# Kernel optimization log

Hardware: AMD Instinct MI355X
Metric: run time of the kernel (lower is better)

Reference implementation:

```python
import jax, jax.numpy as jnp
import numpy as np

B = 32768      # number of sets
N = 131072     # total elements
DIM = 128      # feature dim
HID = 64       # hidden dim
MAXP = 17      # max_n + 1 (one-hot positional dim / size-class count)


def _ln(x, g, b, eps=1e-5):
    m = jnp.mean(x, -1, keepdims=True)
    v = jnp.var(x, -1, keepdims=True)
    return (x - m) * jax.lax.rsqrt(v + eps) * g + b


def _mlp_ln(x, w1, b1, g, bt, w2, b2):
    return jnp.tanh(_ln(x @ w1 + b1, g, bt)) @ w2 + b2


def _mlp(x, w1, b1, w2, b2):
    return jnp.tanh(x @ w1 + b1) @ w2 + b2


def _lin_init(key, fan_in, fan_out):
    k1, k2 = jax.random.split(key)
    s = 1.0 / np.sqrt(fan_in)
    return (jax.random.uniform(k1, (fan_in, fan_out), jnp.float32, -s, s),
            jax.random.uniform(k2, (fan_out,), jnp.float32, -s, s))


def setup_inputs() -> dict:
    key = jax.random.key(0)
    ks = jax.random.split(key, 16)
    inp = {}
    inp['x'] = jax.random.normal(ks[0], (N, DIM), jnp.float32)
    inp['batch'] = jnp.sort(jax.random.randint(ks[1], (N,), 0, B)).astype(jnp.int64)
    # rank: Linear(dim, 1)
    inp['rank_w'], inp['rank_b'] = _lin_init(ks[2], DIM, 1)
    # enc_psi: dim -> 96 -> hid, LayerNorm
    inp['psi_w1'], inp['psi_b1'] = _lin_init(ks[3], DIM, 96)
    inp['psi_g'] = jnp.ones((96,), jnp.float32); inp['psi_bt'] = jnp.zeros((96,), jnp.float32)
    inp['psi_w2'], inp['psi_b2'] = _lin_init(ks[4], 96, HID)
    # encoder pos_encoder: 17 -> 40 -> hid, LayerNorm
    inp['pe_e_w1'], inp['pe_e_b1'] = _lin_init(ks[5], MAXP, 40)
    inp['pe_e_g'] = jnp.ones((40,), jnp.float32); inp['pe_e_bt'] = jnp.zeros((40,), jnp.float32)
    inp['pe_e_w2'], inp['pe_e_b2'] = _lin_init(ks[6], 40, HID)
    # enc_phi: (hid+17)=81 -> 72 -> hid, no LN
    inp['phi_w1'], inp['phi_b1'] = _lin_init(ks[7], HID + MAXP, 72)
    inp['phi_w2'], inp['phi_b2'] = _lin_init(ks[8], 72, HID)
    # size_pred: hid -> 40 -> 17, no LN
    inp['size_w1'], inp['size_b1'] = _lin_init(ks[9], HID, 40)
    inp['size_w2'], inp['size_b2'] = _lin_init(ks[10], 40, MAXP)
    # decoder pos_encoder: 17 -> 40 -> hid, LayerNorm
    inp['pe_d_w1'], inp['pe_d_b1'] = _lin_init(ks[11], MAXP, 40)
    inp['pe_d_g'] = jnp.ones((40,), jnp.float32); inp['pe_d_bt'] = jnp.zeros((40,), jnp.float32)
    inp['pe_d_w2'], inp['pe_d_b2'] = _lin_init(ks[12], 40, HID)
    # decoder: hid -> 96 -> dim, no LN
    inp['dec_w1'], inp['dec_b1'] = _lin_init(ks[13], HID, 96)
    inp['dec_w2'], inp['dec_b2'] = _lin_init(ks[14], 96, DIM)
    return inp


def reference(x, batch, rank_w, rank_b,
              psi_w1, psi_b1, psi_g, psi_bt, psi_w2, psi_b2,
              pe_e_w1, pe_e_b1, pe_e_g, pe_e_bt, pe_e_w2, pe_e_b2,
              phi_w1, phi_b1, phi_w2, phi_b2,
              size_w1, size_b1, size_w2, size_b2,
              pe_d_w1, pe_d_b1, pe_d_g, pe_d_bt, pe_d_w2, pe_d_b2,
              dec_w1, dec_b1, dec_w2, dec_b2):
    batch = batch.astype(jnp.int32)
    # ---- Encoder ----
    n = jax.ops.segment_sum(jnp.ones(N, jnp.int32), batch, num_segments=B)  # [B]
    seg_start = jnp.cumsum(n) - n                                           # ptr[:-1]
    mag = (x @ rank_w + rank_b).reshape(-1)                                 # rank scores
    idx = jnp.lexsort((mag, batch))  # per-segment sort (batch is grouped/sorted)
    xs = x[idx]                                                             # [N, DIM]
    keys = jnp.arange(N) - seg_start[batch]                                 # position in set
    pos = jax.nn.one_hot(keys, MAXP, dtype=x.dtype)                         # [N, MAXP]
    y1 = _mlp_ln(xs, psi_w1, psi_b1, psi_g, psi_bt, psi_w2, psi_b2) * \
         _mlp_ln(pos, pe_e_w1, pe_e_b1, pe_e_g, pe_e_bt, pe_e_w2, pe_e_b2)
    y2 = jax.ops.segment_sum(y1, batch, num_segments=B)                     # [B, HID]
    pos_n = jax.nn.one_hot(n, MAXP, dtype=x.dtype)
    z = _mlp(jnp.concatenate([y2, pos_n], -1), phi_w1, phi_b1, phi_w2, phi_b2)  # [B, HID]
    # ---- Decoder ----
    logits = _mlp(z, size_w1, size_b1, size_w2, size_b2)                    # [B, MAXP]
    n_dec = jnp.argmax(logits, -1)                                          # [B]
    pe = _mlp_ln(jnp.eye(MAXP, dtype=x.dtype),
                 pe_d_w1, pe_d_b1, pe_d_g, pe_d_bt, pe_d_w2, pe_d_b2)       # [MAXP, HID]
    zp = z[:, None, :] * pe[None, :, :]                                     # [B, MAXP, HID]
    xr = _mlp(zp, dec_w1, dec_b1, dec_w2, dec_b2)                           # [B, MAXP, DIM]
    mask = jnp.arange(MAXP)[None, :] < n_dec[:, None]                       # valid slots
    xr = jnp.where(mask[..., None], xr, 0.0)
    batchr = jnp.broadcast_to(jnp.arange(B)[:, None], (B, MAXP))
    return xr.reshape(B * MAXP, DIM), batchr.reshape(-1), mask.reshape(-1)
```

## Files before the change

### kernel.cpp

```cpp
#include <hip/hip_runtime.h>

#define NELEM 131072
#define BSETS 32768
#define DIM 128
#define HID 64
#define MAXP 17

typedef __attribute__((ext_vector_type(8))) short short8;
typedef __attribute__((ext_vector_type(4))) float f32x4;

__device__ __forceinline__ unsigned short f2bf(float f) {
  unsigned u = __float_as_uint(f);
  u += 0x7fff + ((u >> 16) & 1);
  return (unsigned short)(u >> 16);
}

__device__ __forceinline__ float bf2f(unsigned short h) {
  return __uint_as_float((unsigned)h << 16);
}

__device__ __forceinline__ float fast_tanh(float x) {
  float t = __expf(2.0f * x);
  float r = __builtin_amdgcn_rcpf(t + 1.0f);
  return fmaf(-2.0f, r, 1.0f);
}

__device__ void pos_mlp40(int row, const float* w1, const float* b1, const float* g,
                          const float* bt, const float* w2, const float* b2, float* out) {
  float h[40];
  for (int j = 0; j < 40; ++j) h[j] = b1[j] + (row >= 0 ? w1[row * 40 + j] : 0.0f);
  float s = 0.f;
  for (int j = 0; j < 40; ++j) s += h[j];
  float mean = s * (1.0f / 40.0f);
  float v = 0.f;
  for (int j = 0; j < 40; ++j) { float d = h[j] - mean; v += d * d; }
  float rs = rsqrtf(v * (1.0f / 40.0f) + 1e-5f);
  float tb[40];
  for (int j = 0; j < 40; ++j) tb[j] = fast_tanh((h[j] - mean) * rs * g[j] + bt[j]);
  for (int o = 0; o < 64; ++o) {
    float a = b2[o];
    for (int j = 0; j < 40; ++j) a += tb[j] * w2[j * 64 + o];
    out[o] = a;
  }
}

__global__ __launch_bounds__(256) void k_init(
    const float* __restrict__ x, const int* __restrict__ batch,
    const float* __restrict__ rank_w, const float* __restrict__ rank_b,
    double* __restrict__ mag, int* __restrict__ start,
    const float* ew1, const float* eb1, const float* eg, const float* ebt,
    const float* ew2, const float* eb2,
    const float* dw1, const float* db1, const float* dg, const float* dbt,
    const float* dw2, const float* db2,
    float* enc_tab, float* dec_tab,
    const float* __restrict__ decw1, const float* __restrict__ decw2,
    unsigned short* __restrict__ w1s, unsigned short* __restrict__ w2s,
    const float* __restrict__ psiw1, const float* __restrict__ psiw2,
    unsigned short* __restrict__ pw1h, unsigned short* __restrict__ pw1l,
    unsigned short* __restrict__ pw2h, unsigned short* __restrict__ pw2l) {
  int blk = blockIdx.x;
  int t = threadIdx.x;
  if (blk < 1024) {
    int lane = t & 63;
    int w = t >> 6;
    float2 wv = ((const float2*)rank_w)[lane];
    double w0 = wv.x, w1 = wv.y;
    double rb = rank_b[0];
    int rowbase = (blk * 4 + w) * 32;
    for (int it = 0; it < 32; ++it) {
      int row = rowbase + it;
      float2 xv = ((const float2*)(x + (size_t)row * DIM))[lane];
      double acc = (double)xv.x * w0 + (double)xv.y * w1;
#pragma unroll
      for (int m = 1; m < 64; m <<= 1)
        acc += __shfl_xor(acc, m, 64);
      if (lane == 0) mag[row] = acc + rb;
    }
  } else if (blk < 1536) {
    int i = (blk - 1024) * 256 + t;
    int b = batch[i];
    if (i == 0) {
      for (int bb = 0; bb <= b; ++bb) start[bb] = 0;
    } else {
      int bp = batch[i - 1];
      for (int bb = bp + 1; bb <= b; ++bb) start[bb] = i;
    }
    if (i == NELEM - 1) {
      for (int bb = b + 1; bb <= BSETS; ++bb) start[bb] = NELEM;
    }
  } else if (blk == 1536) {
    if (t < 18) {
      float out[64];
      pos_mlp40(t < 17 ? t : -1, ew1, eb1, eg, ebt, ew2, eb2, out);
      for (int o = 0; o < 64; ++o) enc_tab[t * 64 + o] = out[o];
    } else if (t >= 32 && t < 49) {
      float out[64];
      pos_mlp40(t - 32, dw1, db1, dg, dbt, dw2, db2, out);
      for (int o = 0; o < 64; ++o) dec_tab[(t - 32) * 64 + o] = out[o];
    }
  } else {
    int idx = (blk - 1537) * 256 + t;
    if (idx < 6144) {
      int i = idx & 7, lane = (idx >> 3) & 63, rest = idx >> 9;
      int jt = rest % 6, s = rest / 6;
      int k = s * 32 + (lane >> 4) * 8 + i;
      int n = jt * 16 + (lane & 15);
      w1s[idx] = f2bf(decw1[k * 96 + n]);
    }
    int idx2 = idx - 6144;
    if (idx2 >= 0 && idx2 < 12288) {
      int i = idx2 & 7, lane = (idx2 >> 3) & 63, rest = idx2 >> 9;
      int jt = rest % 8, s = rest / 8;
      int k = s * 32 + (lane >> 4) * 8 + i;
      int n = jt * 16 + (lane & 15);
      w2s[idx2] = f2bf(decw2[k * 128 + n]);
    }
    int idx3 = idx - 18432;
    if (idx3 >= 0 && idx3 < 12288) {
      int i = idx3 & 7, lane = (idx3 >> 3) & 63, rest = idx3 >> 9;
      int jt = rest % 6, s = rest / 6;
      int k = s * 32 + (lane >> 4) * 8 + i;
      int n = jt * 16 + (lane & 15);
      float v = psiw1[k * 96 + n];
      unsigned short h = f2bf(v);
      pw1h[idx3] = h;
      pw1l[idx3] = f2bf(v - bf2f(h));
    }
    int idx4 = idx - 30720;
    if (idx4 >= 0 && idx4 < 6144) {
      int i = idx4 & 7, lane = (idx4 >> 3) & 63, rest = idx4 >> 9;
      int nt = rest % 4, s = rest / 4;
      int k = s * 32 + (lane >> 4) * 8 + i;
      int n = nt * 16 + (lane & 15);
      float v = psiw2[k * 64 + n];
      unsigned short h = f2bf(v);
      pw2h[idx4] = h;
      pw2l[idx4] = f2bf(v - bf2f(h));
    }
  }
}

__global__ __launch_bounds__(256) void k_encoder(
    const float* __restrict__ x, const int* __restrict__ batch,
    const double* __restrict__ mag, const int* __restrict__ start,
    const unsigned short* __restrict__ w1h, const unsigned short* __restrict__ w1l,
    const float* __restrict__ b1, const float* __restrict__ g, const float* __restrict__ bt,
    const unsigned short* __restrict__ w2h, const unsigned short* __restrict__ w2l,
    const float* __restrict__ b2,
    const float* __restrict__ enc_tab, float* __restrict__ y1) {
  __shared__ float tt[64][100];
  __shared__ int pos_s[64];
  __shared__ int row_s[64];
  int t = threadIdx.x;
  int lane = t & 63;
  int w = __builtin_amdgcn_readfirstlane(t >> 6);
  int base = blockIdx.x * 64;
  int r = lane & 15, gq = lane >> 4;

  if (w == 0) {
    int gi = base + lane;
    int b = batch[gi];
    int segs = start[b], sege = start[b + 1];
    double mi = mag[gi];
    int kk = 0;
    for (int j = segs; j < sege; ++j) {
      double mj = mag[j];
      kk += (mj < mi) || (mj == mi && j < gi);
    }
    pos_s[lane] = segs + kk;
    row_s[lane] = kk < MAXP ? kk : MAXP;
  }

  const float* xr = x + (size_t)(base + w * 16 + r) * DIM + gq * 8;
  short8 ah[4], al[4];
#pragma unroll
  for (int s = 0; s < 4; ++s) {
    float4 v0 = *(const float4*)(xr + s * 32);
    float4 v1 = *(const float4*)(xr + s * 32 + 4);
    float vv[8] = {v0.x, v0.y, v0.z, v0.w, v1.x, v1.y, v1.z, v1.w};
#pragma unroll
    for (int i = 0; i < 8; ++i) {
      unsigned short h = f2bf(vv[i]);
      ((unsigned short*)&ah[s])[i] = h;
      ((unsigned short*)&al[s])[i] = f2bf(vv[i] - bf2f(h));
    }
  }

  const short8* W1H = (const short8*)w1h;
  const short8* W1L = (const short8*)w1l;
  f32x4 acc1[6] = {};
#pragma unroll
  for (int jt = 0; jt < 6; ++jt) {
#pragma unroll
    for (int s = 0; s < 4; ++s) {
      short8 bh = W1H[(s * 6 + jt) * 64 + lane];
      short8 bl = W1L[(s * 6 + jt) * 64 + lane];
      acc1[jt] = __builtin_amdgcn_mfma_f32_16x16x32_bf16(ah[s], bh, acc1[jt], 0, 0, 0);
      acc1[jt] = __builtin_amdgcn_mfma_f32_16x16x32_bf16(ah[s], bl, acc1[jt], 0, 0, 0);
      acc1[jt] = __builtin_amdgcn_mfma_f32_16x16x32_bf16(al[s], bh, acc1[jt], 0, 0, 0);
    }
  }

  float b1v[6], gv[6], btv[6];
#pragma unroll
  for (int jt = 0; jt < 6; ++jt) {
    b1v[jt] = b1[jt * 16 + r];
    gv[jt] = g[jt * 16 + r];
    btv[jt] = bt[jt * 16 + r];
  }
#pragma unroll
  for (int reg = 0; reg < 4; ++reg) {
    float h[6];
    float s1 = 0.f, s2 = 0.f;
#pragma unroll
    for (int jt = 0; jt < 6; ++jt) {
      h[jt] = acc1[jt][reg] + b1v[jt];
      s1 += h[jt]; s2 += h[jt] * h[jt];
    }
#pragma unroll
    for (int m = 1; m < 16; m <<= 1) {
      s1 += __shfl_xor(s1, m, 64);
      s2 += __shfl_xor(s2, m, 64);
    }
    float mean = s1 * (1.0f / 96.0f);
    float var = s2 * (1.0f / 96.0f) - mean * mean;
    float rs = rsqrtf(var + 1e-5f);
    int rowl = w * 16 + gq * 4 + reg;
#pragma unroll
    for (int jt = 0; jt < 6; ++jt)
      tt[rowl][jt * 16 + r] = fast_tanh((h[jt] - mean) * rs * gv[jt] + btv[jt]);
  }
  __syncthreads();

  const float* trow = &tt[w * 16 + r][0] + gq * 8;
  short8 a2h[3], a2l[3];
#pragma unroll
  for (int s = 0; s < 3; ++s) {
    float4 u0 = *(const float4*)(trow + s * 32);
    float4 u1 = *(const float4*)(trow + s * 32 + 4);
    float vv[8] = {u0.x, u0.y, u0.z, u0.w, u1.x, u1.y, u1.z, u1.w};
#pragma unroll
    for (int i = 0; i < 8; ++i) {
      unsigned short h = f2bf(vv[i]);
      ((unsigned short*)&a2h[s])[i] = h;
      ((unsigned short*)&a2l[s])[i] = f2bf(vv[i] - bf2f(h));
    }
  }

  const short8* W2H = (const short8*)w2h;
  const short8* W2L = (const short8*)w2l;
  f32x4 acc2[4] = {};
#pragma unroll
  for (int nt = 0; nt < 4; ++nt) {
#pragma unroll
    for (int s = 0; s < 3; ++s) {
      short8 bh = W2H[(s * 4 + nt) * 64 + lane];
      short8 bl = W2L[(s * 4 + nt) * 64 + lane];
      acc2[nt] = __builtin_amdgcn_mfma_f32_16x16x32_bf16(a2h[s], bh, acc2[nt], 0, 0, 0);
      acc2[nt] = __builtin_amdgcn_mfma_f32_16x16x32_bf16(a2h[s], bl, acc2[nt], 0, 0, 0);
      acc2[nt] = __builtin_amdgcn_mfma_f32_16x16x32_bf16(a2l[s], bh, acc2[nt], 0, 0, 0);
    }
  }

  float b2v[4];
#pragma unroll
  for (int nt = 0; nt < 4; ++nt) b2v[nt] = b2[nt * 16 + r];
#pragma unroll
  for (int reg = 0; reg < 4; ++reg) {
    int rowl = w * 16 + gq * 4 + reg;
    int pos = pos_s[rowl];
    const float* pe = enc_tab + row_s[rowl] * 64;
    float* yd = y1 + (size_t)pos * 64;
#pragma unroll
    for (int nt = 0; nt < 4; ++nt) {
      int col = nt * 16 + r;
      yd[col] = (acc2[nt][reg] + b2v[nt]) * pe[col];
    }
  }
}

__global__ __launch_bounds__(256) void k_phi(const float* __restrict__ y1,
                                             const int* __restrict__ start,
                                             const float* __restrict__ w1, const float* __restrict__ b1,
                                             const float* __restrict__ w2, const float* __restrict__ b2,
                                             const float* __restrict__ sw1, const float* __restrict__ sb1,
                                             const float* __restrict__ sw2, const float* __restrict__ sb2,
                                             float* __restrict__ z, int* __restrict__ ndec) {
  __shared__ float yt[64][65];
  __shared__ float tt[64][73];
  __shared__ float zt[64][65];
  __shared__ float st[64][41];
  int t = threadIdx.x;
  int base = blockIdx.x * 64;
  {
    int s = t >> 2, c = t & 3;
    int sb = base + s;
    int ps = start[sb], pe = start[sb + 1];
    float acc[16];
#pragma unroll
    for (int i = 0; i < 16; ++i) acc[i] = 0.f;
    for (int p = ps; p < pe; ++p) {
      const float4* row = (const float4*)(y1 + (size_t)p * 64 + c * 16);
#pragma unroll
      for (int q = 0; q < 4; ++q) {
        float4 v = row[q];
        acc[4 * q] += v.x; acc[4 * q + 1] += v.y; acc[4 * q + 2] += v.z; acc[4 * q + 3] += v.w;
      }
    }
#pragma unroll
    for (int i = 0; i < 16; ++i) yt[s][c * 16 + i] = acc[i];
  }
  __syncthreads();
  int lane = t & 63;
  int w = __builtin_amdgcn_readfirstlane(t >> 6);
  int sb = base + lane;
  int nb = start[sb + 1] - start[sb];
  int j0 = w * 18;
  float acc[18];
#pragma unroll
  for (int jj = 0; jj < 18; ++jj) acc[jj] = b1[j0 + jj];
  for (int k = 0; k < 64; ++k) {
    float yv = yt[lane][k];
#pragma unroll
    for (int jj = 0; jj < 18; ++jj) acc[jj] += yv * w1[k * 72 + j0 + jj];
  }
  if (nb < MAXP) {
    const float* wr = w1 + (64 + nb) * 72 + j0;
#pragma unroll
    for (int jj = 0; jj < 18; ++jj) acc[jj] += wr[jj];
  }
#pragma unroll
  for (int jj = 0; jj < 18; ++jj) tt[lane][j0 + jj] = fast_tanh(acc[jj]);
  __syncthreads();
  int o0 = w * 16;
  float acc2[16];
#pragma unroll
  for (int oo = 0; oo < 16; ++oo) acc2[oo] = b2[o0 + oo];
  for (int j = 0; j < 72; ++j) {
    float tv = tt[lane][j];
#pragma unroll
    for (int oo = 0; oo < 16; ++oo) acc2[oo] += tv * w2[j * 64 + o0 + oo];
  }
  float4* zd = (float4*)(z + (size_t)sb * 64 + o0);
#pragma unroll
  for (int q = 0; q < 4; ++q)
    zd[q] = make_float4(acc2[4 * q], acc2[4 * q + 1], acc2[4 * q + 2], acc2[4 * q + 3]);
#pragma unroll
  for (int oo = 0; oo < 16; ++oo) zt[lane][o0 + oo] = acc2[oo];
  __syncthreads();
  int s0 = w * 10;
  float hs[10];
#pragma unroll
  for (int jj = 0; jj < 10; ++jj) hs[jj] = sb1[s0 + jj];
  for (int o = 0; o < 64; ++o) {
    float v = zt[lane][o];
#pragma unroll
    for (int jj = 0; jj < 10; ++jj) hs[jj] += v * sw1[o * 40 + s0 + jj];
  }
#pragma unroll
  for (int jj = 0; jj < 10; ++jj) st[lane][s0 + jj] = fast_tanh(hs[jj]);
  __syncthreads();
  if (w == 0) {
    float lg[17];
#pragma unroll
    for (int l = 0; l < 17; ++l) lg[l] = sb2[l];
    for (int j = 0; j < 40; ++j) {
      float tv = st[lane][j];
#pragma unroll
      for (int l = 0; l < 17; ++l) lg[l] += tv * sw2[j * 17 + l];
    }
    float best = lg[0]; int bi = 0;
#pragma unroll
    for (int l = 1; l < 17; ++l) if (lg[l] > best) { best = lg[l]; bi = l; }
    ndec[sb] = bi;
  }
}

__global__ __launch_bounds__(256) void k_decoder(
    const float* __restrict__ z, const float* __restrict__ dec_tab,
    const unsigned short* __restrict__ w1s, const unsigned short* __restrict__ w2s,
    const float* __restrict__ b1, const float* __restrict__ b2,
    const int* __restrict__ ndec, float* __restrict__ out0,
    float* __restrict__ out1, float* __restrict__ out2) {
  __shared__ __align__(16) unsigned short h2[64][104];
  int t = threadIdx.x;
  int lane = t & 63;
  int w = __builtin_amdgcn_readfirstlane(t >> 6);
  int quad = lane >> 4, m = lane & 15;
  int r = blockIdx.x * 64 + w * 16 + m;
  int b = r / 17, p = r - b * 17;
  const float4* z4 = (const float4*)(z + (size_t)b * 64);
  const float4* p4 = (const float4*)(dec_tab + p * 64);
  short8 a1[2];
#pragma unroll
  for (int s = 0; s < 2; ++s) {
    int q0 = (s * 32 + quad * 8) >> 2;
    float4 za = z4[q0], zb = z4[q0 + 1];
    float4 pa = p4[q0], pb = p4[q0 + 1];
    unsigned short* ap = (unsigned short*)&a1[s];
    ap[0] = f2bf(za.x * pa.x); ap[1] = f2bf(za.y * pa.y);
    ap[2] = f2bf(za.z * pa.z); ap[3] = f2bf(za.w * pa.w);
    ap[4] = f2bf(zb.x * pb.x); ap[5] = f2bf(zb.y * pb.y);
    ap[6] = f2bf(zb.z * pb.z); ap[7] = f2bf(zb.w * pb.w);
  }
  const short8* w1f = (const short8*)w1s;
  f32x4 acc[6] = {};
#pragma unroll
  for (int jt = 0; jt < 6; ++jt) {
    acc[jt] = __builtin_amdgcn_mfma_f32_16x16x32_bf16(a1[0], w1f[jt * 64 + lane], acc[jt], 0, 0, 0);
    acc[jt] = __builtin_amdgcn_mfma_f32_16x16x32_bf16(a1[1], w1f[(6 + jt) * 64 + lane], acc[jt], 0, 0, 0);
  }
#pragma unroll
  for (int jt = 0; jt < 6; ++jt) {
    int col = jt * 16 + m;
    float bias = b1[col];
#pragma unroll
    for (int reg = 0; reg < 4; ++reg) {
      int rl = w * 16 + quad * 4 + reg;
      h2[rl][col] = f2bf(fast_tanh(acc[jt][reg] + bias));
    }
  }
  __syncthreads();
  short8 a2[3];
#pragma unroll
  for (int s = 0; s < 3; ++s)
    a2[s] = *(const short8*)&h2[w * 16 + m][s * 32 + quad * 8];
  const short8* w2f = (const short8*)w2s;
  f32x4 acc2[8] = {};
#pragma unroll
  for (int nt = 0; nt < 8; ++nt) {
#pragma unroll
    for (int s = 0; s < 3; ++s)
      acc2[nt] = __builtin_amdgcn_mfma_f32_16x16x32_bf16(a2[s], w2f[(s * 8 + nt) * 64 + lane], acc2[nt], 0, 0, 0);
  }
  int rgbase = blockIdx.x * 64 + w * 16 + quad * 4;
  bool mk[4];
#pragma unroll
  for (int reg = 0; reg < 4; ++reg) {
    int rg = rgbase + reg;
    int bb = rg / 17, pp = rg - bb * 17;
    mk[reg] = (pp >= ndec[bb]);
  }
#pragma unroll
  for (int nt = 0; nt < 8; ++nt) {
    int n = nt * 16 + m;
    float bias = b2[n];
#pragma unroll
    for (int reg = 0; reg < 4; ++reg) {
      float v = acc2[nt][reg] + bias;
      if (mk[reg]) v = 0.0f;
      out0[(size_t)(rgbase + reg) * 128 + n] = v;
    }
  }
  if (t < 64) {
    int rg = blockIdx.x * 64 + t;
    int bb = rg / 17, pp = rg - bb * 17;
    out1[rg] = (float)bb;
    out2[rg] = (pp < ndec[bb]) ? 1.0f : 0.0f;
  }
}

extern "C" void kernel_launch(void* const* d_in, const int* in_sizes, int n_in,
                              void* d_out, int out_size, void* d_ws, size_t ws_size,
                              hipStream_t stream) {
  const float* x = (const float*)d_in[0];
  const int* batch = (const int*)d_in[1];
  const float* rank_w = (const float*)d_in[2];
  const float* rank_b = (const float*)d_in[3];
  const float* psi_w1 = (const float*)d_in[4];
  const float* psi_b1 = (const float*)d_in[5];
  const float* psi_g = (const float*)d_in[6];
  const float* psi_bt = (const float*)d_in[7];
  const float* psi_w2 = (const float*)d_in[8];
  const float* psi_b2 = (const float*)d_in[9];
  const float* pe_e_w1 = (const float*)d_in[10];
  const float* pe_e_b1 = (const float*)d_in[11];
  const float* pe_e_g = (const float*)d_in[12];
  const float* pe_e_bt = (const float*)d_in[13];
  const float* pe_e_w2 = (const float*)d_in[14];
  const float* pe_e_b2 = (const float*)d_in[15];
  const float* phi_w1 = (const float*)d_in[16];
  const float* phi_b1 = (const float*)d_in[17];
  const float* phi_w2 = (const float*)d_in[18];
  const float* phi_b2 = (const float*)d_in[19];
  const float* size_w1 = (const float*)d_in[20];
  const float* size_b1 = (const float*)d_in[21];
  const float* size_w2 = (const float*)d_in[22];
  const float* size_b2 = (const float*)d_in[23];
  const float* pe_d_w1 = (const float*)d_in[24];
  const float* pe_d_b1 = (const float*)d_in[25];
  const float* pe_d_g = (const float*)d_in[26];
  const float* pe_d_bt = (const float*)d_in[27];
  const float* pe_d_w2 = (const float*)d_in[28];
  const float* pe_d_b2 = (const float*)d_in[29];
  const float* dec_w1 = (const float*)d_in[30];
  const float* dec_b1 = (const float*)d_in[31];
  const float* dec_w2 = (const float*)d_in[32];
  const float* dec_b2 = (const float*)d_in[33];

  char* ws = (char*)d_ws;
  int* start = (int*)(ws);
  double* mag = (double*)(ws + 0x40000);
  float* enc_tab = (float*)(ws + 0x1C0000);
  float* dec_tab = (float*)(ws + 0x1C2000);
  unsigned short* w1s = (unsigned short*)(ws + 0x1C4000);
  unsigned short* w2s = (unsigned short*)(ws + 0x1C8000);
  unsigned short* pw1h = (unsigned short*)(ws + 0x1CE000);
  unsigned short* pw1l = (unsigned short*)(ws + 0x1D4000);
  unsigned short* pw2h = (unsigned short*)(ws + 0x1DA000);
  unsigned short* pw2l = (unsigned short*)(ws + 0x1DD000);
  float* zbuf = (float*)(ws + 0x200000);
  int* ndec = (int*)(ws + 0xA00000);

  float* out0 = (float*)d_out;
  float* out1 = out0 + 71303168;
  float* out2 = out1 + 557056;

  float* y1 = out0;

  k_init<<<1681, 256, 0, stream>>>(x, batch, rank_w, rank_b, mag, start,
                                   pe_e_w1, pe_e_b1, pe_e_g, pe_e_bt, pe_e_w2, pe_e_b2,
                                   pe_d_w1, pe_d_b1, pe_d_g, pe_d_bt, pe_d_w2, pe_d_b2,
                                   enc_tab, dec_tab, dec_w1, dec_w2, w1s, w2s,
                                   psi_w1, psi_w2, pw1h, pw1l, pw2h, pw2l);
  k_encoder<<<2048, 256, 0, stream>>>(x, batch, mag, start, pw1h, pw1l,
                                      psi_b1, psi_g, psi_bt, pw2h, pw2l, psi_b2,
                                      enc_tab, y1);
  k_phi<<<512, 256, 0, stream>>>(y1, start, phi_w1, phi_b1, phi_w2, phi_b2,
                                 size_w1, size_b1, size_w2, size_b2, zbuf, ndec);
  k_decoder<<<8704, 256, 0, stream>>>(zbuf, dec_tab, w1s, w2s, dec_b1, dec_b2, ndec,
                                      out0, out1, out2);
}
```

Before: 570.8 us.

## Fuse rank projection into encoder with halo rows, drop global mag buffer

The per-element rank score (x·rank_w in double) moves out of the init kernel and into the encoder. Each encoder block computes scores for its 64 rows plus a 16-row halo on each side and keeps them in shared memory. This removes a separate full pass over x and the global write and reread of the mag array, and shrinks the init launch. In exchange each block reads 1.5x its rows of x for the projection and does more shuffle reductions. Correctness relies on every set holding at most 16 elements, which matches MAXP.

```diff
diff --git a/kernel.cpp b/kernel.cpp
--- a/kernel.cpp
+++ b/kernel.cpp
@@ -45,9 +45,7 @@
 }
 
 __global__ __launch_bounds__(256) void k_init(
-    const float* __restrict__ x, const int* __restrict__ batch,
-    const float* __restrict__ rank_w, const float* __restrict__ rank_b,
-    double* __restrict__ mag, int* __restrict__ start,
+    const int* __restrict__ batch, int* __restrict__ start,
     const float* ew1, const float* eb1, const float* eg, const float* ebt,
     const float* ew2, const float* eb2,
     const float* dw1, const float* db1, const float* dg, const float* dbt,
@@ -60,24 +58,8 @@
     unsigned short* __restrict__ pw2h, unsigned short* __restrict__ pw2l) {
   int blk = blockIdx.x;
   int t = threadIdx.x;
-  if (blk < 1024) {
-    int lane = t & 63;
-    int w = t >> 6;
-    float2 wv = ((const float2*)rank_w)[lane];
-    double w0 = wv.x, w1 = wv.y;
-    double rb = rank_b[0];
-    int rowbase = (blk * 4 + w) * 32;
-    for (int it = 0; it < 32; ++it) {
-      int row = rowbase + it;
-      float2 xv = ((const float2*)(x + (size_t)row * DIM))[lane];
-      double acc = (double)xv.x * w0 + (double)xv.y * w1;
-#pragma unroll
-      for (int m = 1; m < 64; m <<= 1)
-        acc += __shfl_xor(acc, m, 64);
-      if (lane == 0) mag[row] = acc + rb;
-    }
-  } else if (blk < 1536) {
-    int i = (blk - 1024) * 256 + t;
+  if (blk < 512) {
+    int i = blk * 256 + t;
     int b = batch[i];
     if (i == 0) {
       for (int bb = 0; bb <= b; ++bb) start[bb] = 0;
@@ -88,7 +70,7 @@
     if (i == NELEM - 1) {
       for (int bb = b + 1; bb <= BSETS; ++bb) start[bb] = NELEM;
     }
-  } else if (blk == 1536) {
+  } else if (blk == 512) {
     if (t < 18) {
       float out[64];
       pos_mlp40(t < 17 ? t : -1, ew1, eb1, eg, ebt, ew2, eb2, out);
@@ -99,7 +81,7 @@
       for (int o = 0; o < 64; ++o) dec_tab[(t - 32) * 64 + o] = out[o];
     }
   } else {
-    int idx = (blk - 1537) * 256 + t;
+    int idx = (blk - 513) * 256 + t;
     if (idx < 6144) {
       int i = idx & 7, lane = (idx >> 3) & 63, rest = idx >> 9;
       int jt = rest % 6, s = rest / 6;
@@ -142,29 +124,51 @@
 
 __global__ __launch_bounds__(256) void k_encoder(
     const float* __restrict__ x, const int* __restrict__ batch,
-    const double* __restrict__ mag, const int* __restrict__ start,
+    const float* __restrict__ rank_w, const float* __restrict__ rank_b,
+    const int* __restrict__ start,
     const unsigned short* __restrict__ w1h, const unsigned short* __restrict__ w1l,
     const float* __restrict__ b1, const float* __restrict__ g, const float* __restrict__ bt,
     const unsigned short* __restrict__ w2h, const unsigned short* __restrict__ w2l,
     const float* __restrict__ b2,
     const float* __restrict__ enc_tab, float* __restrict__ y1) {
   __shared__ float tt[64][100];
+  __shared__ double mlds[96];
   __shared__ int pos_s[64];
   __shared__ int row_s[64];
   int t = threadIdx.x;
   int lane = t & 63;
   int w = __builtin_amdgcn_readfirstlane(t >> 6);
   int base = blockIdx.x * 64;
+  int hbase = base - 16;
   int r = lane & 15, gq = lane >> 4;
+
+  {
+    float2 wv = ((const float2*)rank_w)[lane];
+    double w0 = wv.x, w1d = wv.y;
+    double rb = rank_b[0];
+    for (int it = 0; it < 24; ++it) {
+      int hr = w * 24 + it;
+      int row = hbase + hr;
+      if (row >= 0 && row < NELEM) {
+        float2 xv = ((const float2*)(x + (size_t)row * DIM))[lane];
+        double acc = (double)xv.x * w0 + (double)xv.y * w1d;
+#pragma unroll
+        for (int m = 1; m < 64; m <<= 1)
+          acc += __shfl_xor(acc, m, 64);
+        if (lane == 0) mlds[hr] = acc + rb;
+      }
+    }
+  }
+  __syncthreads();
 
   if (w == 0) {
     int gi = base + lane;
     int b = batch[gi];
     int segs = start[b], sege = start[b + 1];
-    double mi = mag[gi];
+    double mi = mlds[gi - hbase];
     int kk = 0;
     for (int j = segs; j < sege; ++j) {
-      double mj = mag[j];
+      double mj = mlds[j - hbase];
       kk += (mj < mi) || (mj == mi && j < gi);
     }
     pos_s[lane] = segs + kk;
@@ -500,7 +504,6 @@
 
   char* ws = (char*)d_ws;
   int* start = (int*)(ws);
-  double* mag = (double*)(ws + 0x40000);
   float* enc_tab = (float*)(ws + 0x1C0000);
   float* dec_tab = (float*)(ws + 0x1C2000);
   unsigned short* w1s = (unsigned short*)(ws + 0x1C4000);
@@ -518,12 +521,12 @@
 
   float* y1 = out0;
 
-  k_init<<<1681, 256, 0, stream>>>(x, batch, rank_w, rank_b, mag, start,
-                                   pe_e_w1, pe_e_b1, pe_e_g, pe_e_bt, pe_e_w2, pe_e_b2,
-                                   pe_d_w1, pe_d_b1, pe_d_g, pe_d_bt, pe_d_w2, pe_d_b2,
-                                   enc_tab, dec_tab, dec_w1, dec_w2, w1s, w2s,
-                                   psi_w1, psi_w2, pw1h, pw1l, pw2h, pw2l);
-  k_encoder<<<2048, 256, 0, stream>>>(x, batch, mag, start, pw1h, pw1l,
+  k_init<<<657, 256, 0, stream>>>(batch, start,
+                                  pe_e_w1, pe_e_b1, pe_e_g, pe_e_bt, pe_e_w2, pe_e_b2,
+                                  pe_d_w1, pe_d_b1, pe_d_g, pe_d_bt, pe_d_w2, pe_d_b2,
+                                  enc_tab, dec_tab, dec_w1, dec_w2, w1s, w2s,
+                                  psi_w1, psi_w2, pw1h, pw1l, pw2h, pw2l);
+  k_encoder<<<2048, 256, 0, stream>>>(x, batch, rank_w, rank_b, start, pw1h, pw1l,
                                       psi_b1, psi_g, psi_bt, pw2h, pw2l, psi_b2,
                                       enc_tab, y1);
   k_phi<<<512, 256, 0, stream>>>(y1, start, phi_w1, phi_b1, phi_w2, phi_b2,
```

Measured after the change: 581.0 us. No clear change (+1.8%).
